# Performance work log

Measured on AMD Instinct MI355X. Metric: run time of the kernel, lower is better.

The kernel has to match this reference:

```python
import jax, jax.numpy as jnp
import numpy as np

N_NODES = 50000
N_EDGES = 800000
D_IN = 128
D_OUT = 128


def setup_inputs() -> dict:
    key = jax.random.key(0)
    ks = jax.random.split(key, 10)
    x = jax.random.normal(ks[0], (N_NODES, D_IN), dtype=jnp.float32)
    src = jax.random.randint(ks[1], (N_EDGES,), 0, N_NODES, dtype=jnp.int32)
    dst = jax.random.randint(ks[2], (N_EDGES,), 0, N_NODES, dtype=jnp.int32)
    s = 1.0 / np.sqrt(D_IN)
    def lin(k, din, dout):
        kw, kb = jax.random.split(k)
        W = jax.random.uniform(kw, (din, dout), minval=-s, maxval=s, dtype=jnp.float32)
        b = jax.random.uniform(kb, (dout,), minval=-s, maxval=s, dtype=jnp.float32)
        return W, b
    W1, b1 = lin(ks[3], D_IN, D_IN)
    W2, b2 = lin(ks[4], D_IN, D_IN)
    W3, b3 = lin(ks[5], D_IN, D_OUT)
    return dict(x=x, W1=W1, b1=b1, W2=W2, b2=b2, W3=W3, b3=b3, src=src, dst=dst)


def reference(x, W1, b1, W2, b2, W3, b3, src, dst):
    n = x.shape[0]
    ones = jnp.ones(src.shape[0], dtype=x.dtype)
    in_deg = jax.ops.segment_sum(ones, dst, num_segments=n)    # [N]
    out_deg = jax.ops.segment_sum(ones, src, num_segments=n)   # [N]

    def sage_gcn(h, W, b):
        # DGL SAGEConv(aggregator_type='gcn'), eval mode (feat_drop = identity):
        # h_neigh = (sum_{j in N(i)} h_j + h_i) / (in_deg_i + 1); out = h_neigh @ W + b
        neigh = jax.ops.segment_sum(h[src], dst, num_segments=n)  # [N, D]
        h_neigh = (neigh + h) / (in_deg + 1.0)[:, None]
        return h_neigh @ W + b

    h = sage_gcn(x, W1, b1)
    h = sage_gcn(h, W2, b2)

    # DGL GraphConv norm='both', allow_zero_in_degree=True:
    # out = D_in^{-1/2} A D_out^{-1/2} h W + b, degrees clamped to >= 1
    norm_out = jnp.clip(out_deg, 1.0) ** -0.5
    norm_in = jnp.clip(in_deg, 1.0) ** -0.5
    hs = h * norm_out[:, None]
    agg = jax.ops.segment_sum(hs[src], dst, num_segments=n)
    out = (agg * norm_in[:, None]) @ W3 + b3
    return out
```

## Files before the change

### kernel.cpp

```cpp
#include <hip/hip_runtime.h>

#define NN 50000
#define NE 800000
#define D 128

#define CH 64
#define EPC (NE / CH)
#define RG 8
#define NPR (NN / RG)
#define CSRCAP (NE + 16 * NN)

typedef short bf16x8 __attribute__((ext_vector_type(8)));
typedef float f32x4 __attribute__((ext_vector_type(4)));


__device__ __forceinline__ unsigned bf16rne(float f) {
  unsigned u = __float_as_uint(f);
  return (u + 0x7fffu + ((u >> 16) & 1u)) >> 16;
}
__device__ __forceinline__ unsigned packbf(float lo, float hi) {
  return bf16rne(lo) | (bf16rne(hi) << 16);
}

__global__ __launch_bounds__(256) void cvtw_kernel(const float* __restrict__ x,
                                                   const float* __restrict__ W1,
                                                   const float* __restrict__ W2,
                                                   const float* __restrict__ W3,
                                                   unsigned short* __restrict__ hbf,
                                                   unsigned short* __restrict__ T1,
                                                   unsigned short* __restrict__ T2,
                                                   unsigned short* __restrict__ T3) {
  int b = blockIdx.x;
  int tid = threadIdx.x;
  if (b < 6250) {
    int i = b * 256 + tid;
    float4 v = ((const float4*)x)[i];
    uint2 p;
    p.x = packbf(v.x, v.y);
    p.y = packbf(v.z, v.w);
    ((uint2*)hbf)[i] = p;
  } else if (b < 6442) {
    int g = b - 6250;
    int w = g >> 6;
    int i = (g & 63) * 256 + tid;
    const float* W = (w == 0) ? W1 : (w == 1) ? W2 : W3;
    unsigned short* T = (w == 0) ? T1 : (w == 1) ? T2 : T3;
    int n = i >> 7, k = i & 127;
    T[n * 128 + k] = (unsigned short)bf16rne(W[k * 128 + n]);
  } else {
    if (tid < 16) ((uint4*)(hbf + (size_t)NN * D))[tid] = make_uint4(0, 0, 0, 0);
  }
}

__global__ __launch_bounds__(1024) void hist_kernel(const int* __restrict__ src,
                                                    const int* __restrict__ dst,
                                                    int* __restrict__ partial_dst,
                                                    int* __restrict__ partial_src) {
  __shared__ int hd[NPR];
  __shared__ int hs[NPR];
  int tid = threadIdx.x;
  int c = blockIdx.x >> 3;
  int r = blockIdx.x & 7;
  int base = r * NPR;
  for (int i = tid; i < NPR; i += 1024) { hd[i] = 0; hs[i] = 0; }
  __syncthreads();
  int e0 = c * EPC;
  for (int i = tid; i < EPC; i += 1024) {
    int d = dst[e0 + i];
    int s = src[e0 + i];
    unsigned dr = (unsigned)(d - base);
    unsigned sr = (unsigned)(s - base);
    if (dr < NPR) atomicAdd(&hd[dr], 1);
    if (sr < NPR) atomicAdd(&hs[sr], 1);
  }
  __syncthreads();
  for (int i = tid; i < NPR; i += 1024) {
    partial_dst[c * NN + base + i] = hd[i];
    partial_src[c * NN + base + i] = hs[i];
  }
}

__device__ __forceinline__ int block_excl_scan(int v, int* wsum) {
  int lane = threadIdx.x & 63;
  int w = threadIdx.x >> 6;
  int incl = v;
#pragma unroll
  for (int off = 1; off < 64; off <<= 1) {
    int t = __shfl_up(incl, off);
    if (lane >= off) incl += t;
  }
  if (lane == 63) wsum[w] = incl;
  __syncthreads();
  int wo = 0;
#pragma unroll
  for (int j = 0; j < 4; ++j)
    if (j < w) wo += wsum[j];
  return wo + incl - v;
}

__global__ __launch_bounds__(256) void degscan_kernel(int* __restrict__ partial_dst,
                                                      const int* __restrict__ partial_src,
                                                      int* __restrict__ degtmp,
                                                      int* __restrict__ deg_out,
                                                      int* __restrict__ row_ptr,
                                                      int* __restrict__ partials, int N) {
  __shared__ int wsum[4];
  int d = blockIdx.x * 256 + threadIdx.x;
  int run = 0;
  if (d < N) {
#pragma unroll
    for (int c = 0; c < CH; ++c) {
      int v = partial_dst[c * NN + d];
      partial_dst[c * NN + d] = run;
      run += v;
    }
    degtmp[d] = run;
    int ro = 0;
#pragma unroll
    for (int c = 0; c < CH; ++c) ro += partial_src[c * NN + d];
    deg_out[d] = ro;
  }
  int pad = (run + 15) & ~15;
  int excl = block_excl_scan(pad, wsum);
  if (d < N) row_ptr[d] = excl;
  if (threadIdx.x == 255) partials[blockIdx.x] = excl + pad;
}

__global__ __launch_bounds__(256) void scan2(int* __restrict__ partials,
                                             int* __restrict__ row_ptr, int nb, int N) {
  __shared__ int wsum[4];
  int v = (threadIdx.x < nb) ? partials[threadIdx.x] : 0;
  int excl = block_excl_scan(v, wsum);
  if (threadIdx.x < nb) partials[threadIdx.x] = excl;
  if (threadIdx.x == nb - 1) row_ptr[N] = excl + v;
}

__global__ __launch_bounds__(256) void scan3(int* __restrict__ row_ptr,
                                             const int* __restrict__ partials, int N) {
  int i = blockIdx.x * 256 + threadIdx.x;
  if (i < N) row_ptr[i] += partials[blockIdx.x];
}

__global__ __launch_bounds__(1024) void fill_kernel(const int* __restrict__ src,
                                                    const int* __restrict__ dst,
                                                    const int* __restrict__ row_ptr,
                                                    const int* __restrict__ partial_dst,
                                                    int* __restrict__ csr_src) {
  __shared__ int cur[NPR];
  int tid = threadIdx.x;
  int c = blockIdx.x >> 3;
  int r = blockIdx.x & 7;
  int base = r * NPR;
  for (int i = tid; i < NPR; i += 1024)
    cur[i] = row_ptr[base + i] + partial_dst[c * NN + base + i];
  __syncthreads();
  int e0 = c * EPC;
  for (int i = tid; i < EPC; i += 1024) {
    int d = dst[e0 + i];
    unsigned dr = (unsigned)(d - base);
    if (dr < NPR) {
      int pos = atomicAdd(&cur[dr], 1);
      csr_src[pos] = src[e0 + i];
    }
  }
}

__global__ __launch_bounds__(256) void pad_kernel(const int* __restrict__ row_ptr,
                                                  const int* __restrict__ degtmp,
                                                  int* __restrict__ csr_src, int N) {
  int i = blockIdx.x * 256 + threadIdx.x;
  if (i >= N) return;
  int s = row_ptr[i] + degtmp[i];
  int e = row_ptr[i + 1];
  for (int j = s; j < e; ++j) csr_src[j] = NN;
}

__device__ __forceinline__ void bacc(float* a, uint4 u) {
  a[0] += __uint_as_float(u.x << 16);
  a[1] += __uint_as_float(u.x & 0xffff0000u);
  a[2] += __uint_as_float(u.y << 16);
  a[3] += __uint_as_float(u.y & 0xffff0000u);
  a[4] += __uint_as_float(u.z << 16);
  a[5] += __uint_as_float(u.z & 0xffff0000u);
  a[6] += __uint_as_float(u.w << 16);
  a[7] += __uint_as_float(u.w & 0xffff0000u);
}

template <int MODE>
__global__ __launch_bounds__(256) void agg_kernel(const unsigned short* __restrict__ hb,
                                                  const int* __restrict__ row_ptr,
                                                  const int* __restrict__ csr_src,
                                                  const int* __restrict__ degtmp,
                                                  unsigned short* __restrict__ outb, int N) {
  int wid = blockIdx.x * 4 + (threadIdx.x >> 6);
  int lane = threadIdx.x & 63;
  if (wid >= N) return;
  int start = row_ptr[wid];
  int iters = (row_ptr[wid + 1] - start) >> 4;
  int q = lane >> 4;
  int col = lane & 15;
  float a0[8] = {0, 0, 0, 0, 0, 0, 0, 0};
  float a1[8] = {0, 0, 0, 0, 0, 0, 0, 0};
  float a2[8] = {0, 0, 0, 0, 0, 0, 0, 0};
  float a3[8] = {0, 0, 0, 0, 0, 0, 0, 0};
  const int* ce = csr_src + start + q;
  for (int it = 0; it < iters; ++it, ce += 16) {
    int i0 = ce[0];
    int i1 = ce[4];
    int i2 = ce[8];
    int i3 = ce[12];
    uint4 u0 = ((const uint4*)(hb + (size_t)i0 * D))[col];
    uint4 u1 = ((const uint4*)(hb + (size_t)i1 * D))[col];
    uint4 u2 = ((const uint4*)(hb + (size_t)i2 * D))[col];
    uint4 u3 = ((const uint4*)(hb + (size_t)i3 * D))[col];
    bacc(a0, u0);
    bacc(a1, u1);
    bacc(a2, u2);
    bacc(a3, u3);
  }
#pragma unroll
  for (int j = 0; j < 8; ++j) a0[j] = (a0[j] + a1[j]) + (a2[j] + a3[j]);
#pragma unroll
  for (int j = 0; j < 8; ++j) {
    a0[j] += __shfl_xor(a0[j], 16);
    a0[j] += __shfl_xor(a0[j], 32);
  }
  int indeg = degtmp[wid];
  if (MODE == 0) {
    uint4 s = ((const uint4*)(hb + (size_t)wid * D))[col];
    float sf[8] = {0, 0, 0, 0, 0, 0, 0, 0};
    bacc(sf, s);
    float inv = 1.0f / (float)(indeg + 1);
#pragma unroll
    for (int j = 0; j < 8; ++j) a0[j] = (a0[j] + sf[j]) * inv;
  } else {
    float sc = rsqrtf(fmaxf((float)indeg, 1.0f));
#pragma unroll
    for (int j = 0; j < 8; ++j) a0[j] *= sc;
  }
  if (q == 0) {
    uint4 p;
    p.x = packbf(a0[0], a0[1]);
    p.y = packbf(a0[2], a0[3]);
    p.z = packbf(a0[4], a0[5]);
    p.w = packbf(a0[6], a0[7]);
    ((uint4*)(outb + (size_t)wid * D))[col] = p;
  }
}

template <int MODE, int OUT_BF>
__global__ __launch_bounds__(256) void mgemm_kernel(const unsigned short* __restrict__ A,
                                                    const unsigned short* __restrict__ WT,
                                                    const float* __restrict__ bias,
                                                    const int* __restrict__ deg_out,
                                                    float* __restrict__ outf,
                                                    unsigned short* __restrict__ outb, int N) {
  __shared__ unsigned short sWT[128 * 136];
  int tid = threadIdx.x;
  for (int g = tid; g < 2048; g += 256) {
    int n = g >> 4, c = g & 15;
    uint4 v = ((const uint4*)WT)[g];
    *(uint4*)&sWT[n * 136 + c * 8] = v;
  }
  int wv = tid >> 6;
  int lane = tid & 63;
  int q = lane >> 4;
  int ln = lane & 15;
  int row0 = blockIdx.x * 64 + wv * 16;
  int arow = row0 + ln;
  if (arow >= N) arow = 0;
  const unsigned short* Ar = A + (size_t)arow * 128 + q * 8;
  bf16x8 af0 = *(const bf16x8*)(Ar + 0);
  bf16x8 af1 = *(const bf16x8*)(Ar + 32);
  bf16x8 af2 = *(const bf16x8*)(Ar + 64);
  bf16x8 af3 = *(const bf16x8*)(Ar + 96);
  f32x4 acc[8];
#pragma unroll
  for (int t = 0; t < 8; ++t) acc[t] = (f32x4){0.f, 0.f, 0.f, 0.f};
  __syncthreads();
#pragma unroll
  for (int t = 0; t < 8; ++t) {
    const unsigned short* Wr = &sWT[(t * 16 + ln) * 136 + q * 8];
    bf16x8 b0 = *(const bf16x8*)(Wr + 0);
    bf16x8 b1 = *(const bf16x8*)(Wr + 32);
    bf16x8 b2 = *(const bf16x8*)(Wr + 64);
    bf16x8 b3 = *(const bf16x8*)(Wr + 96);
    acc[t] = __builtin_amdgcn_mfma_f32_16x16x32_bf16(af0, b0, acc[t], 0, 0, 0);
    acc[t] = __builtin_amdgcn_mfma_f32_16x16x32_bf16(af1, b1, acc[t], 0, 0, 0);
    acc[t] = __builtin_amdgcn_mfma_f32_16x16x32_bf16(af2, b2, acc[t], 0, 0, 0);
    acc[t] = __builtin_amdgcn_mfma_f32_16x16x32_bf16(af3, b3, acc[t], 0, 0, 0);
  }
  float scl[4];
#pragma unroll
  for (int r = 0; r < 4; ++r) {
    scl[r] = 1.0f;
    if (MODE == 1) {
      int row = row0 + q * 4 + r;
      int rr = (row < N) ? row : 0;
      scl[r] = rsqrtf(fmaxf((float)deg_out[rr], 1.0f));
    }
  }
#pragma unroll
  for (int t = 0; t < 8; ++t) {
    float b = bias[t * 16 + ln];
#pragma unroll
    for (int r = 0; r < 4; ++r) {
      int row = row0 + q * 4 + r;
      if (row < N) {
        float v = (acc[t][r] + b) * scl[r];
        if (OUT_BF)
          outb[(size_t)row * 128 + t * 16 + ln] = (unsigned short)bf16rne(v);
        else
          outf[(size_t)row * 128 + t * 16 + ln] = v;
      }
    }
  }
}


extern "C" void kernel_launch(void* const* d_in, const int* in_sizes, int n_in,
                              void* d_out, int out_size, void* d_ws, size_t ws_size,
                              hipStream_t stream) {
  const float* x = (const float*)d_in[0];
  const float* W1 = (const float*)d_in[1];
  const float* b1 = (const float*)d_in[2];
  const float* W2 = (const float*)d_in[3];
  const float* b2 = (const float*)d_in[4];
  const float* W3 = (const float*)d_in[5];
  const float* b3 = (const float*)d_in[6];
  const int* src = (const int*)d_in[7];
  const int* dst = (const int*)d_in[8];
  float* out = (float*)d_out;

  const int N = NN;

  unsigned short* hbf = (unsigned short*)d_ws;
  unsigned short* aggB = hbf + (size_t)(NN + 1) * D;
  unsigned short* WT1 = aggB + (size_t)NN * D;
  unsigned short* WT2 = WT1 + D * D;
  unsigned short* WT3 = WT2 + D * D;
  int* partial_dst = (int*)(WT3 + D * D);
  int* partial_src = partial_dst + (size_t)CH * NN;
  int* degtmp = partial_src + (size_t)CH * NN;
  int* deg_out = degtmp + NN;
  int* row_ptr = deg_out + NN;
  int* partials = row_ptr + NN + 1;
  int* csr_src = partials + 256;

  const int scanBlocks = (N + 255) / 256;

  cvtw_kernel<<<6443, 256, 0, stream>>>(x, W1, W2, W3, hbf, WT1, WT2, WT3);
  hist_kernel<<<CH * RG, 1024, 0, stream>>>(src, dst, partial_dst, partial_src);
  degscan_kernel<<<scanBlocks, 256, 0, stream>>>(partial_dst, partial_src, degtmp,
                                                 deg_out, row_ptr, partials, N);
  scan2<<<1, 256, 0, stream>>>(partials, row_ptr, scanBlocks, N);
  scan3<<<scanBlocks, 256, 0, stream>>>(row_ptr, partials, N);
  fill_kernel<<<CH * RG, 1024, 0, stream>>>(src, dst, row_ptr, partial_dst, csr_src);
  pad_kernel<<<scanBlocks, 256, 0, stream>>>(row_ptr, degtmp, csr_src, N);

  int aggBlocks = (N + 3) / 4;
  int gemmBlocks = (N + 63) / 64;

  agg_kernel<0><<<aggBlocks, 256, 0, stream>>>(hbf, row_ptr, csr_src, degtmp, aggB, N);
  mgemm_kernel<0, 1><<<gemmBlocks, 256, 0, stream>>>(aggB, WT1, b1, deg_out, nullptr, hbf, N);
  agg_kernel<0><<<aggBlocks, 256, 0, stream>>>(hbf, row_ptr, csr_src, degtmp, aggB, N);
  mgemm_kernel<1, 1><<<gemmBlocks, 256, 0, stream>>>(aggB, WT2, b2, deg_out, nullptr, hbf, N);
  agg_kernel<1><<<aggBlocks, 256, 0, stream>>>(hbf, row_ptr, csr_src, degtmp, aggB, N);
  mgemm_kernel<0, 0><<<gemmBlocks, 256, 0, stream>>>(aggB, WT3, b3, deg_out, out, nullptr, N);
}
```

Measured before the change: 272.3 us.

## Drop CSR padding, mask tail edges, and software-pipeline gathers in aggregation

Removes the 16-aligned CSR row padding and the pad kernel. Out-of-range edge slots are now masked to a zero sentinel row inside the aggregation kernel. The aggregation loop is software-pipelined so the next index and row loads are issued before the current rows are accumulated, and a min-blocks launch bound is added. The histogram chunk count is also halved. This trades extra register pressure and a few compare/selects for less CSR traffic, one fewer launch, and better latency hiding of the gathers.

Measured after the change: 282.2 us. +3.6%, slower.

```diff
diff --git a/kernel.cpp b/kernel.cpp
--- a/kernel.cpp
+++ b/kernel.cpp
@@ -4,11 +4,11 @@
 #define NE 800000
 #define D 128
 
-#define CH 64
+#define CH 32
 #define EPC (NE / CH)
 #define RG 8
 #define NPR (NN / RG)
-#define CSRCAP (NE + 16 * NN)
+#define CSRCAP (NE + 64)
 
 typedef short bf16x8 __attribute__((ext_vector_type(8)));
 typedef float f32x4 __attribute__((ext_vector_type(4)));
@@ -120,10 +120,9 @@
     for (int c = 0; c < CH; ++c) ro += partial_src[c * NN + d];
     deg_out[d] = ro;
   }
-  int pad = (run + 15) & ~15;
-  int excl = block_excl_scan(pad, wsum);
+  int excl = block_excl_scan(run, wsum);
   if (d < N) row_ptr[d] = excl;
-  if (threadIdx.x == 255) partials[blockIdx.x] = excl + pad;
+  if (threadIdx.x == 255) partials[blockIdx.x] = excl + run;
 }
 
 __global__ __launch_bounds__(256) void scan2(int* __restrict__ partials,
@@ -165,16 +164,6 @@
   }
 }
 
-__global__ __launch_bounds__(256) void pad_kernel(const int* __restrict__ row_ptr,
-                                                  const int* __restrict__ degtmp,
-                                                  int* __restrict__ csr_src, int N) {
-  int i = blockIdx.x * 256 + threadIdx.x;
-  if (i >= N) return;
-  int s = row_ptr[i] + degtmp[i];
-  int e = row_ptr[i + 1];
-  for (int j = s; j < e; ++j) csr_src[j] = NN;
-}
-
 __device__ __forceinline__ void bacc(float* a, uint4 u) {
   a[0] += __uint_as_float(u.x << 16);
   a[1] += __uint_as_float(u.x & 0xffff0000u);
@@ -187,37 +176,67 @@
 }
 
 template <int MODE>
-__global__ __launch_bounds__(256) void agg_kernel(const unsigned short* __restrict__ hb,
-                                                  const int* __restrict__ row_ptr,
-                                                  const int* __restrict__ csr_src,
-                                                  const int* __restrict__ degtmp,
-                                                  unsigned short* __restrict__ outb, int N) {
+__global__ __launch_bounds__(256, 4) void agg_kernel(const unsigned short* __restrict__ hb,
+                                                     const int* __restrict__ row_ptr,
+                                                     const int* __restrict__ csr_src,
+                                                     const int* __restrict__ degtmp,
+                                                     unsigned short* __restrict__ outb, int N) {
   int wid = blockIdx.x * 4 + (threadIdx.x >> 6);
   int lane = threadIdx.x & 63;
   if (wid >= N) return;
   int start = row_ptr[wid];
-  int iters = (row_ptr[wid + 1] - start) >> 4;
+  int deg = degtmp[wid];
+  int iters = (deg + 15) >> 4;
   int q = lane >> 4;
   int col = lane & 15;
+  int dq = deg - q;
+  const int* cp = csr_src + start + q;
   float a0[8] = {0, 0, 0, 0, 0, 0, 0, 0};
   float a1[8] = {0, 0, 0, 0, 0, 0, 0, 0};
   float a2[8] = {0, 0, 0, 0, 0, 0, 0, 0};
   float a3[8] = {0, 0, 0, 0, 0, 0, 0, 0};
-  const int* ce = csr_src + start + q;
-  for (int it = 0; it < iters; ++it, ce += 16) {
-    int i0 = ce[0];
-    int i1 = ce[4];
-    int i2 = ce[8];
-    int i3 = ce[12];
-    uint4 u0 = ((const uint4*)(hb + (size_t)i0 * D))[col];
-    uint4 u1 = ((const uint4*)(hb + (size_t)i1 * D))[col];
-    uint4 u2 = ((const uint4*)(hb + (size_t)i2 * D))[col];
-    uint4 u3 = ((const uint4*)(hb + (size_t)i3 * D))[col];
-    bacc(a0, u0);
-    bacc(a1, u1);
-    bacc(a2, u2);
-    bacc(a3, u3);
-  }
+
+  int n0 = NN, n1 = NN, n2 = NN, n3 = NN;
+  uint4 c0 = make_uint4(0, 0, 0, 0), c1 = c0, c2 = c0, c3 = c0;
+
+  auto loadidx = [&](int T) {
+    int o = T * 16;
+    int t0 = cp[o];
+    int t1 = cp[o + 4];
+    int t2 = cp[o + 8];
+    int t3 = cp[o + 12];
+    n0 = (o < dq) ? t0 : NN;
+    n1 = (o + 4 < dq) ? t1 : NN;
+    n2 = (o + 8 < dq) ? t2 : NN;
+    n3 = (o + 12 < dq) ? t3 : NN;
+  };
+  auto loadrow = [&]() {
+    c0 = ((const uint4*)(hb + (size_t)n0 * D))[col];
+    c1 = ((const uint4*)(hb + (size_t)n1 * D))[col];
+    c2 = ((const uint4*)(hb + (size_t)n2 * D))[col];
+    c3 = ((const uint4*)(hb + (size_t)n3 * D))[col];
+  };
+
+  if (iters > 0) {
+    loadidx(0);
+    loadrow();
+    if (iters > 1) loadidx(1);
+#pragma unroll 1
+    for (int t = 0; t + 1 < iters; ++t) {
+      uint4 p0 = c0, p1 = c1, p2 = c2, p3 = c3;
+      loadrow();
+      if (t + 2 < iters) loadidx(t + 2);
+      bacc(a0, p0);
+      bacc(a1, p1);
+      bacc(a2, p2);
+      bacc(a3, p3);
+    }
+    bacc(a0, c0);
+    bacc(a1, c1);
+    bacc(a2, c2);
+    bacc(a3, c3);
+  }
+
 #pragma unroll
   for (int j = 0; j < 8; ++j) a0[j] = (a0[j] + a1[j]) + (a2[j] + a3[j]);
 #pragma unroll
@@ -225,16 +244,15 @@
     a0[j] += __shfl_xor(a0[j], 16);
     a0[j] += __shfl_xor(a0[j], 32);
   }
-  int indeg = degtmp[wid];
   if (MODE == 0) {
     uint4 s = ((const uint4*)(hb + (size_t)wid * D))[col];
     float sf[8] = {0, 0, 0, 0, 0, 0, 0, 0};
     bacc(sf, s);
-    float inv = 1.0f / (float)(indeg + 1);
+    float inv = 1.0f / (float)(deg + 1);
 #pragma unroll
     for (int j = 0; j < 8; ++j) a0[j] = (a0[j] + sf[j]) * inv;
   } else {
-    float sc = rsqrtf(fmaxf((float)indeg, 1.0f));
+    float sc = rsqrtf(fmaxf((float)deg, 1.0f));
 #pragma unroll
     for (int j = 0; j < 8; ++j) a0[j] *= sc;
   }
@@ -356,7 +374,6 @@
   scan2<<<1, 256, 0, stream>>>(partials, row_ptr, scanBlocks, N);
   scan3<<<scanBlocks, 256, 0, stream>>>(row_ptr, partials, N);
   fill_kernel<<<CH * RG, 1024, 0, stream>>>(src, dst, row_ptr, partial_dst, csr_src);
-  pad_kernel<<<scanBlocks, 256, 0, stream>>>(row_ptr, degtmp, csr_src, N);
 
   int aggBlocks = (N + 3) / 4;
   int gemmBlocks = (N + 63) / 64;
```
